# Optimization experiments

Measured on AMD Instinct MI355X. Metric: run time of the kernel, lower is better.

Reference implementation:

```python
import jax, jax.numpy as jnp
import numpy as np

N, D_IN, D_C, D_Q, K = 4096, 64, 32, 128, 3


def setup_inputs() -> dict:
    key = jax.random.key(0)
    ks = jax.random.split(key, 16)
    rn = lambda k, shp, s: jax.random.normal(k, shp, dtype=jnp.float32) * s
    inp = {
        "x": rn(ks[0], (N, D_IN), 1.0),
        "comms": rn(ks[1], (N, D_C), 0.1),
        # dense positive transition matrix (all entries nonzero -> the
        # trans==0 -> -inf masking step is a faithful no-op here)
        "trans": jax.random.uniform(ks[2], (N, N), dtype=jnp.float32, minval=0.01, maxval=1.0),
        "mask": jnp.ones((N,), dtype=jnp.int32),
        # encoding: Linear(num_inputs + comm_channels, ch_q)
        "W_enc": rn(ks[3], (D_IN + D_C, D_Q), 1.0 / np.sqrt(D_IN + D_C)),
        "b_enc": rn(ks[4], (D_Q,), 0.01),
        # att_decoding[k]: Linear(ch_q, ch_q)
        "W_ad": rn(ks[5], (K, D_Q, D_Q), 1.0 / np.sqrt(D_Q)),
        "b_ad": rn(ks[6], (K, D_Q), 0.01),
        # att[k]: Linear(2*ch_q, 1)
        "w_att": rn(ks[7], (K, 2 * D_Q), 1.0 / np.sqrt(2 * D_Q)),
        "b_att": rn(ks[8], (K,), 0.01),
        # att_vectors[k]: Linear(ch_q, ch_q)
        "W_av": rn(ks[9], (K, D_Q, D_Q), 1.0 / np.sqrt(D_Q)),
        "b_av": rn(ks[10], (K, D_Q), 0.01),
        # decoding: Linear(ch_q, 1)
        "W_dec": rn(ks[11], (D_Q,), 1.0 / np.sqrt(D_Q)),
        "b_dec": rn(ks[12], (), 0.01),
    }
    return inp


def reference(x, comms, trans, mask, W_enc, b_enc, W_ad, b_ad, w_att, b_att,
              W_av, b_av, W_dec, b_dec):
    dq = W_ad.shape[-1]
    # encoding of [node features, communication vector]
    h = jnp.concatenate([x, comms], axis=-1) @ W_enc + b_enc          # (n, dq)
    # trans.transpose(0,1); zeros -> -inf (additive log-mask)
    tb = trans.T
    tb = jnp.where(tb == 0, -jnp.inf, tb)                              # (n, n)
    for k in range(K):
        att = h @ W_ad[k] + b_ad[k]                                    # (n, dq)
        # concat-GAT score: score[i,j] = w_a . att[j] + w_b . att[i] + b
        # (decomposition of Linear(cat(att_t, att_t^T)) -> avoids n x n x 2dq)
        wa, wb = w_att[k, :dq], w_att[k, dq:]
        score = (att @ wb)[:, None] + (att @ wa)[None, :] + b_att[k]   # (n, n)
        focus = jax.nn.softmax(score + tb, axis=1)                     # (n, n)
        v = h @ W_av[k] + b_av[k]                                      # (n, dq)
        h = focus @ v                                                  # (n, dq)
    out = h @ W_dec + b_dec                                            # (n,)
    # final masking (args.rl = False branch): masked nodes -> -inf
    s = out + jnp.where(mask == 0, -jnp.inf, 0.0).astype(out.dtype)
    return s
```

## Files before the change

kernel.cpp:

```cpp
#include <hip/hip_runtime.h>
#include <math.h>

#define N 4096
#define DQ 128
#define DIN 64
#define DC 32
#define NT 9
#define PSTRIDE 144
#define NIT 256
#define LDSF (NT * 512)

typedef __attribute__((ext_vector_type(8))) short short8;
typedef __attribute__((ext_vector_type(8))) _Float16 half8;
typedef __attribute__((ext_vector_type(4))) float f32x4;

__device__ __forceinline__ unsigned short f2h(float x) {
  return __builtin_bit_cast(unsigned short, (_Float16)x);
}
__device__ __forceinline__ void async16(unsigned short* lds, const unsigned short* g) {
  __builtin_amdgcn_global_load_lds(
      (const __attribute__((address_space(1))) void*)g,
      (__attribute__((address_space(3))) void*)lds, 16, 0, 0);
}

__global__ __launch_bounds__(256) void kExp(const float* __restrict__ trans,
                                            unsigned short* __restrict__ Ef) {
  __shared__ float sh[32 * 65];
  const int tid = threadIdx.x;
  const int ig = blockIdx.x;
  const int kt = blockIdx.y;
  const int r = tid >> 3;
  const int c8 = (tid & 7) * 8;
  const float* src = &trans[((size_t)kt * 32 + r) * N + ig * 64 + c8];
  const float4 v0 = *(const float4*)src;
  const float4 v1 = *(const float4*)(src + 4);
  float* d = &sh[r * 65 + c8];
  d[0] = __expf(v0.x); d[1] = __expf(v0.y); d[2] = __expf(v0.z); d[3] = __expf(v0.w);
  d[4] = __expf(v1.x); d[5] = __expf(v1.y); d[6] = __expf(v1.z); d[7] = __expf(v1.w);
  __syncthreads();
  const int itl = tid >> 6;
  const int lane = tid & 63;
  const int quad = lane >> 4, l15 = lane & 15;
  const int col = itl * 16 + l15;
  unsigned short hb[8];
#pragma unroll
  for (int jj = 0; jj < 8; ++jj) hb[jj] = f2h(sh[(quad * 8 + jj) * 65 + col]);
  const short8 s = {(short)hb[0], (short)hb[1], (short)hb[2], (short)hb[3],
                    (short)hb[4], (short)hb[5], (short)hb[6], (short)hb[7]};
  *(short8*)(Ef + (((size_t)kt * NIT + ig * 4 + itl) * 64 + lane) * 8) = s;
}

__device__ __forceinline__ void v_phase(const float* hs_row, float p,
    const float* __restrict__ W_av_k, const float* __restrict__ b_av_k,
    int r, int d4, unsigned short* shh, unsigned short* shl) {
  float a[4] = {b_av_k[d4], b_av_k[d4 + 1], b_av_k[d4 + 2], b_av_k[d4 + 3]};
  for (int c = 0; c < DQ; ++c) {
    const float hv = hs_row[c];
    const float4 w = *(const float4*)&W_av_k[c * DQ + d4];
    a[0] += hv * w.x; a[1] += hv * w.y; a[2] += hv * w.z; a[3] += hv * w.w;
  }
  const int nt = d4 >> 4;
#pragma unroll
  for (int e = 0; e < 4; ++e) {
    const float val = p * a[e];
    const _Float16 hi = (_Float16)val;
    const _Float16 lo = (_Float16)(val - (float)hi);
    const int ix = nt * 128 + ((d4 + e) & 15) * 8 + r;
    shh[ix] = __builtin_bit_cast(unsigned short, hi);
    shl[ix] = __builtin_bit_cast(unsigned short, lo);
  }
  const int c32 = d4 >> 2;
  if (c32 < 16) {
    const int ix = 8 * 128 + c32 * 8 + r;
    if (c32 == 0) {
      const _Float16 phi = (_Float16)p;
      const _Float16 plo = (_Float16)(p - (float)phi);
      shh[ix] = __builtin_bit_cast(unsigned short, phi);
      shl[ix] = __builtin_bit_cast(unsigned short, plo);
    } else {
      shh[ix] = 0; shl[ix] = 0;
    }
  }
}

__device__ __forceinline__ void v_store(int tid, int blk,
    const unsigned short* shh, const unsigned short* shl,
    unsigned short* __restrict__ Vhi, unsigned short* __restrict__ Vlo) {
  const int kt = blk >> 2, quad = blk & 3;
  if (tid < NT * 16) {
    const int nt = tid >> 4, l15 = tid & 15;
    const size_t dst = (((size_t)kt * NT + nt) * 64 + quad * 16 + l15) * 8;
    *(short8*)(Vhi + dst) = *(const short8*)&shh[nt * 128 + l15 * 8];
    *(short8*)(Vlo + dst) = *(const short8*)&shl[nt * 128 + l15 * 8];
  }
}

__global__ __launch_bounds__(256) void kVS0(const float* __restrict__ x,
    const float* __restrict__ comms, const float* __restrict__ W_enc,
    const float* __restrict__ b_enc, const float* __restrict__ W_ad_k,
    const float* __restrict__ wa, const float* __restrict__ W_av_k,
    const float* __restrict__ b_av_k,
    unsigned short* __restrict__ Vhi, unsigned short* __restrict__ Vlo) {
  __shared__ float xs[8][96];
  __shared__ float hs[8][DQ];
  __shared__ float u[DQ];
  __shared__ float pb[8];
  __shared__ __align__(16) unsigned short shh[NT * 128];
  __shared__ __align__(16) unsigned short shl[NT * 128];
  const int tid = threadIdx.x;
  const int blk = blockIdx.x;
  if (tid < 128) {
    const float4 v = *(const float4*)&x[(size_t)blk * 8 * DIN + tid * 4];
    const int idx = tid * 4, r = idx >> 6, c = idx & 63;
    xs[r][c] = v.x; xs[r][c + 1] = v.y; xs[r][c + 2] = v.z; xs[r][c + 3] = v.w;
  } else if (tid < 192) {
    const int t = tid - 128;
    const float4 v = *(const float4*)&comms[(size_t)blk * 8 * DC + t * 4];
    const int idx = t * 4, r = idx >> 5, c = idx & 31;
    xs[r][64 + c] = v.x; xs[r][64 + c + 1] = v.y; xs[r][64 + c + 2] = v.z; xs[r][64 + c + 3] = v.w;
  }
  if (tid < DQ) {
    float s = 0.f;
    const float* wrow = &W_ad_k[tid * DQ];
    for (int q = 0; q < DQ; ++q) s += wrow[q] * wa[q];
    u[tid] = s;
  }
  __syncthreads();
  const int r = tid >> 5;
  const int c32 = tid & 31;
  const int d4 = c32 * 4;
  {
    float a0 = b_enc[d4], a1 = b_enc[d4 + 1], a2 = b_enc[d4 + 2], a3 = b_enc[d4 + 3];
    for (int c = 0; c < 96; ++c) {
      const float hv = xs[r][c];
      const float4 w = *(const float4*)&W_enc[c * DQ + d4];
      a0 += hv * w.x; a1 += hv * w.y; a2 += hv * w.z; a3 += hv * w.w;
    }
    hs[r][d4] = a0; hs[r][d4 + 1] = a1; hs[r][d4 + 2] = a2; hs[r][d4 + 3] = a3;
  }
  __syncthreads();
  float part = 0.f;
  for (int c = c32; c < DQ; c += 32) part += hs[r][c] * u[c];
#pragma unroll
  for (int m = 16; m > 0; m >>= 1) part += __shfl_xor(part, m, 32);
  if (c32 == 0) pb[r] = __expf(part);
  __syncthreads();
  v_phase(hs[r], pb[r], W_av_k, b_av_k, r, d4, shh, shl);
  __syncthreads();
  v_store(tid, blk, shh, shl, Vhi, Vlo);
}

__global__ __launch_bounds__(256) void kVSR(const float* __restrict__ P,
    const float* __restrict__ W_ad_k, const float* __restrict__ wa,
    const float* __restrict__ W_av_k, const float* __restrict__ b_av_k,
    unsigned short* __restrict__ Vhi, unsigned short* __restrict__ Vlo,
    int ksplit) {
  __shared__ float hs[8][DQ];
  __shared__ float u[DQ];
  __shared__ float pb[8];
  __shared__ __align__(16) unsigned short shh[NT * 128];
  __shared__ __align__(16) unsigned short shl[NT * 128];
  const int tid = threadIdx.x;
  const int r = tid >> 5;
  const int c32 = tid & 31;
  const int d4 = c32 * 4;
  const int j = blockIdx.x * 8 + r;
  if (tid < DQ) {
    float s = 0.f;
    const float* wrow = &W_ad_k[tid * DQ];
    for (int q = 0; q < DQ; ++q) s += wrow[q] * wa[q];
    u[tid] = s;
  }
  float4 num = {0.f, 0.f, 0.f, 0.f};
  float den = 0.f;
  for (int s = 0; s < ksplit; ++s) {
    const float* b = &P[((size_t)s * N + j) * PSTRIDE];
    const float4 v = *(const float4*)&b[d4];
    num.x += v.x; num.y += v.y; num.z += v.z; num.w += v.w;
    den += b[128];
  }
  const float inv = 1.f / den;
  hs[r][d4] = num.x * inv; hs[r][d4 + 1] = num.y * inv;
  hs[r][d4 + 2] = num.z * inv; hs[r][d4 + 3] = num.w * inv;
  __syncthreads();
  float part = 0.f;
  for (int c = c32; c < DQ; c += 32) part += hs[r][c] * u[c];
#pragma unroll
  for (int m = 16; m > 0; m >>= 1) part += __shfl_xor(part, m, 32);
  if (c32 == 0) pb[r] = __expf(part);
  __syncthreads();
  v_phase(hs[r], pb[r], W_av_k, b_av_k, r, d4, shh, shl);
  __syncthreads();
  v_store(tid, blockIdx.x, shh, shl, Vhi, Vlo);
}

__global__ __launch_bounds__(256) void kGemm(
    const unsigned short* __restrict__ Ef,
    const unsigned short* __restrict__ Vhi, const unsigned short* __restrict__ Vlo,
    float* __restrict__ P, int nsteps) {
  __shared__ __align__(16) unsigned short ldsB[2][2 * LDSF];
  const int tid = threadIdx.x;
  const int w = tid >> 6, lane = tid & 63;
  const int quad = lane >> 4, l15 = lane & 15;
  const int it0 = blockIdx.x * 8 + w * 2;
  const size_t kt0 = (size_t)blockIdx.y * nsteps;

#pragma unroll
  for (int c = w; c < 2 * NT; c += 4) {
    const unsigned short* g = (c < NT)
        ? Vhi + (kt0 * NT + c) * 512 + lane * 8
        : Vlo + (kt0 * NT + (c - NT)) * 512 + lane * 8;
    async16(&ldsB[0][c * 512], g);
  }
  half8 Ah[2];
#pragma unroll
  for (int ti = 0; ti < 2; ++ti)
    Ah[ti] = __builtin_bit_cast(half8,
        *(const short8*)(Ef + ((kt0 * NIT + it0 + ti) * 64 + lane) * 8));
  f32x4 acc[2][NT];
#pragma unroll
  for (int ti = 0; ti < 2; ++ti)
#pragma unroll
    for (int nt = 0; nt < NT; ++nt) acc[ti][nt] = (f32x4){0.f, 0.f, 0.f, 0.f};
  __syncthreads();

  for (int t = 0; t < nsteps; ++t) {
    const bool more = (t + 1 < nsteps);
    half8 nAh[2];
    if (more) {
      const size_t ktn = kt0 + t + 1;
#pragma unroll
      for (int c = w; c < 2 * NT; c += 4) {
        const unsigned short* g = (c < NT)
            ? Vhi + (ktn * NT + c) * 512 + lane * 8
            : Vlo + (ktn * NT + (c - NT)) * 512 + lane * 8;
        async16(&ldsB[(t + 1) & 1][c * 512], g);
      }
#pragma unroll
      for (int ti = 0; ti < 2; ++ti)
        nAh[ti] = __builtin_bit_cast(half8,
            *(const short8*)(Ef + ((ktn * NIT + it0 + ti) * 64 + lane) * 8));
    }
    const unsigned short* bb = ldsB[t & 1];
#pragma unroll
    for (int nt = 0; nt < NT; ++nt) {
      const half8 Bh = __builtin_bit_cast(half8, *(const short8*)(bb + nt * 512 + lane * 8));
      const half8 Bl = __builtin_bit_cast(half8, *(const short8*)(bb + LDSF + nt * 512 + lane * 8));
      acc[0][nt] = __builtin_amdgcn_mfma_f32_16x16x32_f16(Ah[0], Bh, acc[0][nt], 0, 0, 0);
      acc[0][nt] = __builtin_amdgcn_mfma_f32_16x16x32_f16(Ah[0], Bl, acc[0][nt], 0, 0, 0);
      acc[1][nt] = __builtin_amdgcn_mfma_f32_16x16x32_f16(Ah[1], Bh, acc[1][nt], 0, 0, 0);
      acc[1][nt] = __builtin_amdgcn_mfma_f32_16x16x32_f16(Ah[1], Bl, acc[1][nt], 0, 0, 0);
    }
    if (more) {
      Ah[0] = nAh[0]; Ah[1] = nAh[1];
      __syncthreads();
    }
  }
  float* Pb = P + (size_t)blockIdx.y * N * PSTRIDE;
#pragma unroll
  for (int ti = 0; ti < 2; ++ti) {
#pragma unroll
    for (int nt = 0; nt < NT; ++nt) {
#pragma unroll
      for (int r = 0; r < 4; ++r) {
        const int i = (it0 + ti) * 16 + quad * 4 + r;
        Pb[(size_t)i * PSTRIDE + nt * 16 + l15] = acc[ti][nt][r];
      }
    }
  }
}

__global__ __launch_bounds__(256) void kOutR(const float* __restrict__ P,
    const float* __restrict__ W_dec, const float* __restrict__ b_dec,
    const int* __restrict__ mask, float* __restrict__ out, int ksplit) {
  __shared__ float red[256];
  const int tid = threadIdx.x;
  const int d = tid & 127;
  const int i = blockIdx.x * 2 + (tid >> 7);
  float num = 0.f, den = 0.f;
  for (int s = 0; s < ksplit; ++s) {
    const float* b = &P[((size_t)s * N + i) * PSTRIDE];
    num += b[d];
    den += b[128];
  }
  red[tid] = num * W_dec[d];
  __syncthreads();
  for (int st = 64; st > 0; st >>= 1) {
    if (d < st) red[tid] += red[tid + st];
    __syncthreads();
  }
  if (d == 0) out[i] = (mask[i] == 0) ? -INFINITY : red[tid] / den + b_dec[0];
}

extern "C" void kernel_launch(void* const* d_in, const int* in_sizes, int n_in,
                              void* d_out, int out_size, void* d_ws, size_t ws_size,
                              hipStream_t stream) {
  (void)in_sizes; (void)n_in; (void)out_size;
  const float* x     = (const float*)d_in[0];
  const float* comms = (const float*)d_in[1];
  const float* trans = (const float*)d_in[2];
  const int*   mask  = (const int*)d_in[3];
  const float* W_enc = (const float*)d_in[4];
  const float* b_enc = (const float*)d_in[5];
  const float* W_ad  = (const float*)d_in[6];
  const float* w_att = (const float*)d_in[8];
  const float* W_av  = (const float*)d_in[10];
  const float* b_av  = (const float*)d_in[11];
  const float* W_dec = (const float*)d_in[12];
  const float* b_dec = (const float*)d_in[13];
  float* out         = (float*)d_out;

  char* ws = (char*)d_ws;
  unsigned short* Vhi = (unsigned short*)ws;  ws += (size_t)N * PSTRIDE * 2;
  unsigned short* Vlo = (unsigned short*)ws;  ws += (size_t)N * PSTRIDE * 2;
  unsigned short* Ef  = (unsigned short*)ws;  ws += (size_t)N * N * 2;
  float* P = (float*)ws;
  const size_t fixedB = (size_t)N * PSTRIDE * 4 + (size_t)N * N * 2;
  const size_t perB   = (size_t)N * PSTRIDE * 4;
  const int ksplit = (ws_size >= fixedB + 16 * perB) ? 16 : 8;
  const int nsteps = (N / ksplit) >> 5;

  kExp<<<dim3(64, 128), 256, 0, stream>>>(trans, Ef);
  for (int k = 0; k < 3; ++k) {
    const float* W_ad_k = W_ad + (size_t)k * DQ * DQ;
    const float* wa     = w_att + (size_t)k * 2 * DQ;
    const float* W_av_k = W_av + (size_t)k * DQ * DQ;
    const float* b_av_k = b_av + (size_t)k * DQ;
    if (k == 0) {
      kVS0<<<N / 8, 256, 0, stream>>>(x, comms, W_enc, b_enc, W_ad_k, wa,
                                      W_av_k, b_av_k, Vhi, Vlo);
    } else {
      kVSR<<<N / 8, 256, 0, stream>>>(P, W_ad_k, wa, W_av_k, b_av_k,
                                      Vhi, Vlo, ksplit);
    }
    kGemm<<<dim3(NIT / 8, ksplit), 256, 0, stream>>>(Ef, Vhi, Vlo, P, nsteps);
  }
  kOutR<<<N / 2, 256, 0, stream>>>(P, W_dec, b_dec, mask, out, ksplit);
}
```

Before: 245.9 us.

## Drop split-fp16 V, fold decoder into last layer, shrink GEMM blocks

Removes the hi/lo fp16 split of the V operand, so each GEMM does one MFMA per tile instead of two and loads half the B data. For the last layer it projects V onto W_dec before the attention GEMM, so that GEMM has one output column tile instead of nine, and the output kernel becomes a simple per-row divide. GEMM blocks go from 256 to 128 threads with half the row tiles each. Dropping the lo correction loses precision in V, since fp16 rounding now applies to p·v directly.

```diff
diff --git a/kernel.cpp b/kernel.cpp
--- a/kernel.cpp
+++ b/kernel.cpp
@@ -6,9 +6,9 @@
 #define DIN 64
 #define DC 32
 #define NT 9
-#define PSTRIDE 144
+#define PST9 144
+#define PST1 16
 #define NIT 256
-#define LDSF (NT * 512)
 
 typedef __attribute__((ext_vector_type(8))) short short8;
 typedef __attribute__((ext_vector_type(8))) _Float16 half8;
@@ -52,7 +52,7 @@
 
 __device__ __forceinline__ void v_phase(const float* hs_row, float p,
     const float* __restrict__ W_av_k, const float* __restrict__ b_av_k,
-    int r, int d4, unsigned short* shh, unsigned short* shl) {
+    int r, int d4, unsigned short* shh) {
   float a[4] = {b_av_k[d4], b_av_k[d4 + 1], b_av_k[d4 + 2], b_av_k[d4 + 3]};
   for (int c = 0; c < DQ; ++c) {
     const float hv = hs_row[c];
@@ -61,37 +61,20 @@
   }
   const int nt = d4 >> 4;
 #pragma unroll
-  for (int e = 0; e < 4; ++e) {
-    const float val = p * a[e];
-    const _Float16 hi = (_Float16)val;
-    const _Float16 lo = (_Float16)(val - (float)hi);
-    const int ix = nt * 128 + ((d4 + e) & 15) * 8 + r;
-    shh[ix] = __builtin_bit_cast(unsigned short, hi);
-    shl[ix] = __builtin_bit_cast(unsigned short, lo);
-  }
+  for (int e = 0; e < 4; ++e)
+    shh[nt * 128 + ((d4 + e) & 15) * 8 + r] = f2h(p * a[e]);
   const int c32 = d4 >> 2;
-  if (c32 < 16) {
-    const int ix = 8 * 128 + c32 * 8 + r;
-    if (c32 == 0) {
-      const _Float16 phi = (_Float16)p;
-      const _Float16 plo = (_Float16)(p - (float)phi);
-      shh[ix] = __builtin_bit_cast(unsigned short, phi);
-      shl[ix] = __builtin_bit_cast(unsigned short, plo);
-    } else {
-      shh[ix] = 0; shl[ix] = 0;
-    }
-  }
+  if (c32 < 16)
+    shh[8 * 128 + c32 * 8 + r] = (c32 == 0) ? f2h(p) : 0;
 }
 
 __device__ __forceinline__ void v_store(int tid, int blk,
-    const unsigned short* shh, const unsigned short* shl,
-    unsigned short* __restrict__ Vhi, unsigned short* __restrict__ Vlo) {
+    const unsigned short* shh, unsigned short* __restrict__ Vf) {
   const int kt = blk >> 2, quad = blk & 3;
   if (tid < NT * 16) {
     const int nt = tid >> 4, l15 = tid & 15;
     const size_t dst = (((size_t)kt * NT + nt) * 64 + quad * 16 + l15) * 8;
-    *(short8*)(Vhi + dst) = *(const short8*)&shh[nt * 128 + l15 * 8];
-    *(short8*)(Vlo + dst) = *(const short8*)&shl[nt * 128 + l15 * 8];
+    *(short8*)(Vf + dst) = *(const short8*)&shh[nt * 128 + l15 * 8];
   }
 }
 
@@ -99,14 +82,12 @@
     const float* __restrict__ comms, const float* __restrict__ W_enc,
     const float* __restrict__ b_enc, const float* __restrict__ W_ad_k,
     const float* __restrict__ wa, const float* __restrict__ W_av_k,
-    const float* __restrict__ b_av_k,
-    unsigned short* __restrict__ Vhi, unsigned short* __restrict__ Vlo) {
+    const float* __restrict__ b_av_k, unsigned short* __restrict__ Vf) {
   __shared__ float xs[8][96];
   __shared__ float hs[8][DQ];
   __shared__ float u[DQ];
   __shared__ float pb[8];
   __shared__ __align__(16) unsigned short shh[NT * 128];
-  __shared__ __align__(16) unsigned short shl[NT * 128];
   const int tid = threadIdx.x;
   const int blk = blockIdx.x;
   if (tid < 128) {
@@ -145,21 +126,19 @@
   for (int m = 16; m > 0; m >>= 1) part += __shfl_xor(part, m, 32);
   if (c32 == 0) pb[r] = __expf(part);
   __syncthreads();
-  v_phase(hs[r], pb[r], W_av_k, b_av_k, r, d4, shh, shl);
-  __syncthreads();
-  v_store(tid, blk, shh, shl, Vhi, Vlo);
+  v_phase(hs[r], pb[r], W_av_k, b_av_k, r, d4, shh);
+  __syncthreads();
+  v_store(tid, blk, shh, Vf);
 }
 
 __global__ __launch_bounds__(256) void kVSR(const float* __restrict__ P,
     const float* __restrict__ W_ad_k, const float* __restrict__ wa,
     const float* __restrict__ W_av_k, const float* __restrict__ b_av_k,
-    unsigned short* __restrict__ Vhi, unsigned short* __restrict__ Vlo,
-    int ksplit) {
+    unsigned short* __restrict__ Vf, int ksplit) {
   __shared__ float hs[8][DQ];
   __shared__ float u[DQ];
   __shared__ float pb[8];
   __shared__ __align__(16) unsigned short shh[NT * 128];
-  __shared__ __align__(16) unsigned short shl[NT * 128];
   const int tid = threadIdx.x;
   const int r = tid >> 5;
   const int c32 = tid & 31;
@@ -174,7 +153,7 @@
   float4 num = {0.f, 0.f, 0.f, 0.f};
   float den = 0.f;
   for (int s = 0; s < ksplit; ++s) {
-    const float* b = &P[((size_t)s * N + j) * PSTRIDE];
+    const float* b = &P[((size_t)s * N + j) * PST9];
     const float4 v = *(const float4*)&b[d4];
     num.x += v.x; num.y += v.y; num.z += v.z; num.w += v.w;
     den += b[128];
@@ -189,39 +168,89 @@
   for (int m = 16; m > 0; m >>= 1) part += __shfl_xor(part, m, 32);
   if (c32 == 0) pb[r] = __expf(part);
   __syncthreads();
-  v_phase(hs[r], pb[r], W_av_k, b_av_k, r, d4, shh, shl);
-  __syncthreads();
-  v_store(tid, blockIdx.x, shh, shl, Vhi, Vlo);
-}
-
-__global__ __launch_bounds__(256) void kGemm(
-    const unsigned short* __restrict__ Ef,
-    const unsigned short* __restrict__ Vhi, const unsigned short* __restrict__ Vlo,
+  v_phase(hs[r], pb[r], W_av_k, b_av_k, r, d4, shh);
+  __syncthreads();
+  v_store(tid, blockIdx.x, shh, Vf);
+}
+
+__global__ __launch_bounds__(256) void kVSRc(const float* __restrict__ P,
+    const float* __restrict__ W_ad_k, const float* __restrict__ wa,
+    const float* __restrict__ W_av_k, const float* __restrict__ b_av_k,
+    const float* __restrict__ W_dec, unsigned short* __restrict__ Vc,
+    int ksplit) {
+  __shared__ float hs[8][DQ];
+  __shared__ float u[DQ];
+  __shared__ float pb[8];
+  const int tid = threadIdx.x;
+  const int r = tid >> 5;
+  const int c32 = tid & 31;
+  const int d4 = c32 * 4;
+  const int j = blockIdx.x * 8 + r;
+  if (tid < DQ) {
+    float s = 0.f;
+    const float* wrow = &W_ad_k[tid * DQ];
+    for (int q = 0; q < DQ; ++q) s += wrow[q] * wa[q];
+    u[tid] = s;
+  }
+  float4 num = {0.f, 0.f, 0.f, 0.f};
+  float den = 0.f;
+  for (int s = 0; s < ksplit; ++s) {
+    const float* b = &P[((size_t)s * N + j) * PST9];
+    const float4 v = *(const float4*)&b[d4];
+    num.x += v.x; num.y += v.y; num.z += v.z; num.w += v.w;
+    den += b[128];
+  }
+  const float inv = 1.f / den;
+  hs[r][d4] = num.x * inv; hs[r][d4 + 1] = num.y * inv;
+  hs[r][d4 + 2] = num.z * inv; hs[r][d4 + 3] = num.w * inv;
+  __syncthreads();
+  float part = 0.f;
+  for (int c = c32; c < DQ; c += 32) part += hs[r][c] * u[c];
+#pragma unroll
+  for (int m = 16; m > 0; m >>= 1) part += __shfl_xor(part, m, 32);
+  if (c32 == 0) pb[r] = __expf(part);
+  __syncthreads();
+  float a[4] = {b_av_k[d4], b_av_k[d4 + 1], b_av_k[d4 + 2], b_av_k[d4 + 3]};
+  for (int c = 0; c < DQ; ++c) {
+    const float hv = hs[r][c];
+    const float4 w = *(const float4*)&W_av_k[c * DQ + d4];
+    a[0] += hv * w.x; a[1] += hv * w.y; a[2] += hv * w.z; a[3] += hv * w.w;
+  }
+  float vd = a[0] * W_dec[d4] + a[1] * W_dec[d4 + 1]
+           + a[2] * W_dec[d4 + 2] + a[3] * W_dec[d4 + 3];
+#pragma unroll
+  for (int m = 16; m > 0; m >>= 1) vd += __shfl_xor(vd, m, 32);
+  const float p = pb[r];
+  if (c32 < 16) {
+    const int blk = blockIdx.x;
+    const size_t ix = (((size_t)(blk >> 2)) * 64 + (blk & 3) * 16 + c32) * 8 + r;
+    Vc[ix] = (c32 == 0) ? f2h(p * vd) : (c32 == 1) ? f2h(p) : 0;
+  }
+}
+
+template <int NTT, int PST>
+__global__ __launch_bounds__(128) void kGemm(
+    const unsigned short* __restrict__ Ef, const unsigned short* __restrict__ Vf,
     float* __restrict__ P, int nsteps) {
-  __shared__ __align__(16) unsigned short ldsB[2][2 * LDSF];
+  __shared__ __align__(16) unsigned short ldsB[2][NTT * 512];
   const int tid = threadIdx.x;
   const int w = tid >> 6, lane = tid & 63;
   const int quad = lane >> 4, l15 = lane & 15;
-  const int it0 = blockIdx.x * 8 + w * 2;
+  const int it0 = blockIdx.x * 4 + w * 2;
   const size_t kt0 = (size_t)blockIdx.y * nsteps;
 
-#pragma unroll
-  for (int c = w; c < 2 * NT; c += 4) {
-    const unsigned short* g = (c < NT)
-        ? Vhi + (kt0 * NT + c) * 512 + lane * 8
-        : Vlo + (kt0 * NT + (c - NT)) * 512 + lane * 8;
-    async16(&ldsB[0][c * 512], g);
-  }
+  for (int c = w; c < NTT; c += 2)
+    async16(&ldsB[0][c * 512], Vf + (kt0 * NTT + c) * 512 + lane * 8);
   half8 Ah[2];
 #pragma unroll
   for (int ti = 0; ti < 2; ++ti)
     Ah[ti] = __builtin_bit_cast(half8,
         *(const short8*)(Ef + ((kt0 * NIT + it0 + ti) * 64 + lane) * 8));
-  f32x4 acc[2][NT];
+  f32x4 acc[2][NTT];
 #pragma unroll
   for (int ti = 0; ti < 2; ++ti)
 #pragma unroll
-    for (int nt = 0; nt < NT; ++nt) acc[ti][nt] = (f32x4){0.f, 0.f, 0.f, 0.f};
+    for (int nt = 0; nt < NTT; ++nt) acc[ti][nt] = (f32x4){0.f, 0.f, 0.f, 0.f};
   __syncthreads();
 
   for (int t = 0; t < nsteps; ++t) {
@@ -229,13 +258,8 @@
     half8 nAh[2];
     if (more) {
       const size_t ktn = kt0 + t + 1;
-#pragma unroll
-      for (int c = w; c < 2 * NT; c += 4) {
-        const unsigned short* g = (c < NT)
-            ? Vhi + (ktn * NT + c) * 512 + lane * 8
-            : Vlo + (ktn * NT + (c - NT)) * 512 + lane * 8;
-        async16(&ldsB[(t + 1) & 1][c * 512], g);
-      }
+      for (int c = w; c < NTT; c += 2)
+        async16(&ldsB[(t + 1) & 1][c * 512], Vf + (ktn * NTT + c) * 512 + lane * 8);
 #pragma unroll
       for (int ti = 0; ti < 2; ++ti)
         nAh[ti] = __builtin_bit_cast(half8,
@@ -243,53 +267,41 @@
     }
     const unsigned short* bb = ldsB[t & 1];
 #pragma unroll
-    for (int nt = 0; nt < NT; ++nt) {
+    for (int nt = 0; nt < NTT; ++nt) {
       const half8 Bh = __builtin_bit_cast(half8, *(const short8*)(bb + nt * 512 + lane * 8));
-      const half8 Bl = __builtin_bit_cast(half8, *(const short8*)(bb + LDSF + nt * 512 + lane * 8));
       acc[0][nt] = __builtin_amdgcn_mfma_f32_16x16x32_f16(Ah[0], Bh, acc[0][nt], 0, 0, 0);
-      acc[0][nt] = __builtin_amdgcn_mfma_f32_16x16x32_f16(Ah[0], Bl, acc[0][nt], 0, 0, 0);
       acc[1][nt] = __builtin_amdgcn_mfma_f32_16x16x32_f16(Ah[1], Bh, acc[1][nt], 0, 0, 0);
-      acc[1][nt] = __builtin_amdgcn_mfma_f32_16x16x32_f16(Ah[1], Bl, acc[1][nt], 0, 0, 0);
     }
     if (more) {
       Ah[0] = nAh[0]; Ah[1] = nAh[1];
       __syncthreads();
     }
   }
-  float* Pb = P + (size_t)blockIdx.y * N * PSTRIDE;
+  float* Pb = P + (size_t)blockIdx.y * N * PST;
 #pragma unroll
   for (int ti = 0; ti < 2; ++ti) {
 #pragma unroll
-    for (int nt = 0; nt < NT; ++nt) {
+    for (int nt = 0; nt < NTT; ++nt) {
 #pragma unroll
       for (int r = 0; r < 4; ++r) {
         const int i = (it0 + ti) * 16 + quad * 4 + r;
-        Pb[(size_t)i * PSTRIDE + nt * 16 + l15] = acc[ti][nt][r];
+        Pb[(size_t)i * PST + nt * 16 + l15] = acc[ti][nt][r];
       }
     }
   }
 }
 
-__global__ __launch_bounds__(256) void kOutR(const float* __restrict__ P,
-    const float* __restrict__ W_dec, const float* __restrict__ b_dec,
-    const int* __restrict__ mask, float* __restrict__ out, int ksplit) {
-  __shared__ float red[256];
-  const int tid = threadIdx.x;
-  const int d = tid & 127;
-  const int i = blockIdx.x * 2 + (tid >> 7);
+__global__ __launch_bounds__(256) void kOut(const float* __restrict__ P3,
+    const float* __restrict__ b_dec, const int* __restrict__ mask,
+    float* __restrict__ out, int ksplit) {
+  const int i = blockIdx.x * 256 + threadIdx.x;
   float num = 0.f, den = 0.f;
   for (int s = 0; s < ksplit; ++s) {
-    const float* b = &P[((size_t)s * N + i) * PSTRIDE];
-    num += b[d];
-    den += b[128];
-  }
-  red[tid] = num * W_dec[d];
-  __syncthreads();
-  for (int st = 64; st > 0; st >>= 1) {
-    if (d < st) red[tid] += red[tid + st];
-    __syncthreads();
-  }
-  if (d == 0) out[i] = (mask[i] == 0) ? -INFINITY : red[tid] / den + b_dec[0];
+    const float* b = &P3[((size_t)s * N + i) * PST1];
+    num += b[0];
+    den += b[1];
+  }
+  out[i] = (mask[i] == 0) ? -INFINITY : num / den + b_dec[0];
 }
 
 extern "C" void kernel_launch(void* const* d_in, const int* in_sizes, int n_in,
@@ -311,29 +323,31 @@
   float* out         = (float*)d_out;
 
   char* ws = (char*)d_ws;
-  unsigned short* Vhi = (unsigned short*)ws;  ws += (size_t)N * PSTRIDE * 2;
-  unsigned short* Vlo = (unsigned short*)ws;  ws += (size_t)N * PSTRIDE * 2;
-  unsigned short* Ef  = (unsigned short*)ws;  ws += (size_t)N * N * 2;
-  float* P = (float*)ws;
-  const size_t fixedB = (size_t)N * PSTRIDE * 4 + (size_t)N * N * 2;
-  const size_t perB   = (size_t)N * PSTRIDE * 4;
+  unsigned short* Vf = (unsigned short*)ws;  ws += (size_t)(N / 32) * NT * 512 * 2;
+  unsigned short* Vc = (unsigned short*)ws;  ws += (size_t)(N / 32) * 512 * 2;
+  unsigned short* Ef = (unsigned short*)ws;  ws += (size_t)N * N * 2;
+  float* P  = (float*)ws;
+  const size_t fixedB = (size_t)(N / 32) * (NT + 1) * 1024 + (size_t)N * N * 2;
+  const size_t perB   = (size_t)N * (PST9 + PST1) * 4;
   const int ksplit = (ws_size >= fixedB + 16 * perB) ? 16 : 8;
+  float* P3 = P + (size_t)ksplit * N * PST9;
   const int nsteps = (N / ksplit) >> 5;
 
   kExp<<<dim3(64, 128), 256, 0, stream>>>(trans, Ef);
-  for (int k = 0; k < 3; ++k) {
-    const float* W_ad_k = W_ad + (size_t)k * DQ * DQ;
-    const float* wa     = w_att + (size_t)k * 2 * DQ;
-    const float* W_av_k = W_av + (size_t)k * DQ * DQ;
-    const float* b_av_k = b_av + (size_t)k * DQ;
-    if (k == 0) {
-      kVS0<<<N / 8, 256, 0, stream>>>(x, comms, W_enc, b_enc, W_ad_k, wa,
-                                      W_av_k, b_av_k, Vhi, Vlo);
-    } else {
-      kVSR<<<N / 8, 256, 0, stream>>>(P, W_ad_k, wa, W_av_k, b_av_k,
-                                      Vhi, Vlo, ksplit);
-    }
-    kGemm<<<dim3(NIT / 8, ksplit), 256, 0, stream>>>(Ef, Vhi, Vlo, P, nsteps);
-  }
-  kOutR<<<N / 2, 256, 0, stream>>>(P, W_dec, b_dec, mask, out, ksplit);
-}
+  const float* wa1 = w_att;
+  kVS0<<<N / 8, 256, 0, stream>>>(x, comms, W_enc, b_enc, W_ad, wa1,
+                                  W_av, b_av, Vf);
+  kGemm<NT, PST9><<<dim3(NIT / 4, ksplit), 128, 0, stream>>>(Ef, Vf, P, nsteps);
+
+  kVSR<<<N / 8, 256, 0, stream>>>(P, W_ad + (size_t)1 * DQ * DQ,
+                                  w_att + 2 * DQ, W_av + (size_t)1 * DQ * DQ,
+                                  b_av + DQ, Vf, ksplit);
+  kGemm<NT, PST9><<<dim3(NIT / 4, ksplit), 128, 0, stream>>>(Ef, Vf, P, nsteps);
+
+  kVSRc<<<N / 8, 256, 0, stream>>>(P, W_ad + (size_t)2 * DQ * DQ,
+                                   w_att + 4 * DQ, W_av + (size_t)2 * DQ * DQ,
+                                   b_av + 2 * DQ, W_dec, Vc, ksplit);
+  kGemm<1, PST1><<<dim3(NIT / 4, ksplit), 128, 0, stream>>>(Ef, Vc, P3, nsteps);
+
+  kOut<<<N / 256, 256, 0, stream>>>(P3, b_dec, mask, out, ksplit);
+}
```

Measured after the change: 227.5 us. -7.5%, faster.
